# Kernel optimization log

Hardware: AMD Instinct MI355X
Metric: run time of the kernel (lower is better)

## Reference

```python
import jax, jax.numpy as jnp
import numpy as np
import math

HW = (14, 14)          # spatial token grid
L = HW[0] * HW[1]      # 196 spatial tokens
NUM_HEADS = 12
HEAD_DIM = 64
DIM = NUM_HEADS * HEAD_DIM
STEP_LEN = 4           # extension mode: 4 directions, step_length-1 = 3 entries
NUM_DIR = 4
NUM_ENTRY = STEP_LEN - 1
DE = NUM_DIR * NUM_ENTRY  # 12 table channels


def build_spatial_table() -> np.ndarray:
    """Dense [L, L, NUM_DIR*NUM_ENTRY] aggregation table (extension mode)."""
    Hh, Ww = HW
    table = np.zeros((L, L, DE), dtype=np.float32)
    for rank in range(L):
        h, w = divmod(rank, Ww)
        for step in range(1, STEP_LEN):
            dist = math.exp(-step ** 2 / STEP_LEN ** 2)
            se = step - 1
            top = rank - step * Ww
            bottom = rank + step * Ww
            left = rank - step
            right = rank + step
            if top >= 0:
                table[rank, top, 0 * NUM_ENTRY + se] = dist
            if bottom < L:
                table[rank, bottom, 1 * NUM_ENTRY + se] = dist
            if left >= 0 and left // Ww == h:
                table[rank, left, 2 * NUM_ENTRY + se] = dist
            if right < L and right // Ww == h:
                table[rank, right, 3 * NUM_ENTRY + se] = dist
    return table


def setup_inputs() -> dict:
    key = jax.random.key(0)
    ks = jax.random.split(key, 8)
    B, N = 64, L + 1  # +1 class token (skip=1)
    s_in = 1.0 / math.sqrt(DIM)
    inp = {
        "x": jax.random.normal(ks[0], (B, N, DIM), jnp.float32),
        "qkv_w": jax.random.normal(ks[1], (DIM, 3 * DIM), jnp.float32) * s_in,
        "qkv_b": jnp.zeros((3 * DIM,), jnp.float32),
        "proj_w": jax.random.normal(ks[2], (DIM, DIM), jnp.float32) * s_in,
        "proj_b": jnp.zeros((DIM,), jnp.float32),
        "wq": jax.random.normal(ks[3], (DE, NUM_HEADS), jnp.float32) * 0.02,
        "wk": jax.random.normal(ks[4], (DE, NUM_HEADS), jnp.float32) * 0.02,
        "wv": jax.random.normal(ks[5], (DE, NUM_HEADS), jnp.float32) * 0.02,
        "spatial_table": jnp.asarray(build_spatial_table()),
    }
    return inp


def _save_aggregate(v, table, w):
    """SAVE aggregation for one of q/k/v.

    v: [B, H, N, hd] with class token at position 0 (skipped).
    table: [L, L, DE] sparse positional aggregation weights.
    w: [DE, H] per-head channel mixing weights.
    Anchor buffer is identity -> residual add of the spatial tokens.
    """
    cls_tok, sp = v[:, :, :1, :], v[:, :, 1:, :]        # [B,H,1,hd], [B,H,L,hd]
    table_h = jnp.einsum('ije,eh->hij', table, w)       # [H, L, L]
    agg = sp + jnp.einsum('hij,bhjd->bhid', table_h, sp)
    return jnp.concatenate([cls_tok, agg], axis=2)


def reference(x, qkv_w, qkv_b, proj_w, proj_b, wq, wk, wv, spatial_table):
    B, N, C = x.shape
    H, hd = NUM_HEADS, HEAD_DIM
    scale = hd ** -0.5
    qkv = (x @ qkv_w + qkv_b).reshape(B, N, 3, H, hd)
    q, k, v = (jnp.transpose(qkv[:, :, i], (0, 2, 1, 3)) for i in range(3))  # [B,H,N,hd]
    q = _save_aggregate(q, spatial_table, wq)
    k = _save_aggregate(k, spatial_table, wk)
    v = _save_aggregate(v, spatial_table, wv)
    attn = jax.nn.softmax(jnp.einsum('bhid,bhjd->bhij', q, k) * scale, axis=-1)
    out = jnp.einsum('bhij,bhjd->bhid', attn, v)        # [B,H,N,hd]
    out = jnp.transpose(out, (0, 2, 1, 3)).reshape(B, N, C)
    return out @ proj_w + proj_b
```

## Files before the change

### kernel.cpp

```cpp
#include <hip/hip_runtime.h>

typedef unsigned short u16;
typedef __attribute__((ext_vector_type(8))) short short8;
typedef __attribute__((ext_vector_type(4))) float f32x4;

__device__ __forceinline__ u16 f2bf(float f) {
  unsigned u = __builtin_bit_cast(unsigned, f);
  u += 0x7FFFu + ((u >> 16) & 1u);
  return (u16)(u >> 16);
}
__device__ __forceinline__ float bf2f(u16 s) {
  unsigned u = ((unsigned)s) << 16;
  return __builtin_bit_cast(float, u);
}
__device__ __forceinline__ void gll16(const u16* g, u16* l) {
  __builtin_amdgcn_global_load_lds(
      (const __attribute__((address_space(1))) void*)g,
      (__attribute__((address_space(3))) void*)l, 16, 0, 0);
}

__global__ __launch_bounds__(256) void convert_f32_bf16(
    const float* __restrict__ in, u16* __restrict__ out, int n4) {
  int i = blockIdx.x * 256 + threadIdx.x;
  if (i >= n4) return;
  float4 v = ((const float4*)in)[i];
  ushort4 o;
  o.x = f2bf(v.x); o.y = f2bf(v.y); o.z = f2bf(v.z); o.w = f2bf(v.w);
  ((ushort4*)out)[i] = o;
}

__global__ __launch_bounds__(256) void transpose_f32_bf16(
    const float* __restrict__ in, u16* __restrict__ out, int R, int C) {
  __shared__ float tile[32][33];
  int c0 = blockIdx.x * 32, r0 = blockIdx.y * 32;
  int tx = threadIdx.x, ty = threadIdx.y;
  #pragma unroll
  for (int i = 0; i < 32; i += 8)
    tile[ty + i][tx] = in[(size_t)(r0 + ty + i) * C + c0 + tx];
  __syncthreads();
  #pragma unroll
  for (int i = 0; i < 32; i += 8)
    out[(size_t)(c0 + ty + i) * R + r0 + tx] = f2bf(tile[tx][ty + i]);
}

template<int MODE>
__global__ __launch_bounds__(256) void gemm_gll(
    const u16* __restrict__ A, const u16* __restrict__ Bt, int M, int NT,
    const float* __restrict__ bias, u16* __restrict__ ob, float* __restrict__ of) {
  constexpr int K = 768;
  __shared__ __align__(16) u16 Al[128 * 32];
  __shared__ __align__(16) u16 Bl[128 * 32];
  int tid = threadIdx.x, lane = tid & 63, w = tid >> 6;
  int nwg = gridDim.x, orig = blockIdx.x;
  int q = nwg >> 3, r = nwg & 7, xcd = orig & 7, slot = orig >> 3;
  int wg = (xcd < r ? xcd * (q + 1) : r * (q + 1) + (xcd - r) * q) + slot;
  int mt = wg / NT, nt = wg - mt * NT;
  int m0 = mt * 128, n0 = nt * 128;
  int wm = w >> 1, wn = w & 1;
  int lq = lane & 15, oct = lane >> 4;
  int srow = lane >> 2;
  int scol = (lane & 3) << 3;
  int ar0 = m0 + w * 16 + srow;      if (ar0 > M - 1) ar0 = M - 1;
  int ar1 = m0 + 64 + w * 16 + srow; if (ar1 > M - 1) ar1 = M - 1;
  const u16* ga0 = A + (size_t)ar0 * K + scol;
  const u16* ga1 = A + (size_t)ar1 * K + scol;
  const u16* gb0 = Bt + (size_t)(n0 + w * 16 + srow) * K + scol;
  const u16* gb1 = Bt + (size_t)(n0 + 64 + w * 16 + srow) * K + scol;
  u16* la0 = Al + w * 512;
  u16* la1 = Al + 2048 + w * 512;
  u16* lb0 = Bl + w * 512;
  u16* lb1 = Bl + 2048 + w * 512;
  f32x4 acc[4][4] = {};
  for (int kt = 0; kt < K; kt += 32) {
    gll16(ga0 + kt, la0);
    gll16(ga1 + kt, la1);
    gll16(gb0 + kt, lb0);
    gll16(gb1 + kt, lb1);
    __syncthreads();
    short8 af[4], bq[4];
    #pragma unroll
    for (int i = 0; i < 4; ++i)
      af[i] = *(const short8*)(Al + (wm * 64 + i * 16 + lq) * 32 + oct * 8);
    #pragma unroll
    for (int j = 0; j < 4; ++j)
      bq[j] = *(const short8*)(Bl + (wn * 64 + j * 16 + lq) * 32 + oct * 8);
    #pragma unroll
    for (int i = 0; i < 4; ++i)
      #pragma unroll
      for (int j = 0; j < 4; ++j)
        acc[i][j] = __builtin_amdgcn_mfma_f32_16x16x32_bf16(af[i], bq[j], acc[i][j], 0, 0, 0);
    __syncthreads();
  }
  int ldc = NT * 128;
  float bs[4];
  #pragma unroll
  for (int j = 0; j < 4; ++j) bs[j] = bias[n0 + wn * 64 + j * 16 + lq];
  #pragma unroll
  for (int i = 0; i < 4; ++i) {
    #pragma unroll
    for (int rr = 0; rr < 4; ++rr) {
      int m = m0 + wm * 64 + i * 16 + oct * 4 + rr;
      if (m < M) {
        #pragma unroll
        for (int j = 0; j < 4; ++j) {
          int c = n0 + wn * 64 + j * 16 + lq;
          float val = acc[i][j][rr] + bs[j];
          if (MODE == 0) ob[(size_t)m * ldc + c] = f2bf(val);
          else           of[(size_t)m * ldc + c] = val;
        }
      }
    }
  }
}

__global__ __launch_bounds__(256) void save_agg_fused(
    const u16* __restrict__ in, u16* __restrict__ q2, u16* __restrict__ k2,
    u16* __restrict__ v2, const float* __restrict__ wq,
    const float* __restrict__ wk, const float* __restrict__ wv) {
  constexpr int PER = 768 * 197 * 8;
  int vid = blockIdx.x * 256 + threadIdx.x;
  if (vid >= 3 * PER) return;
  int which = vid / PER;
  int rem = vid - which * PER;
  int dv = rem & 7;
  int n = (rem >> 3) % 197;
  int bh = rem / (197 * 8);
  int b = bh / 12, h = bh - b * 12;
  const float* w = (which == 0) ? wq : (which == 1) ? wk : wv;
  u16* outp = (which == 0) ? q2 : (which == 1) ? k2 : v2;
  size_t colbase = (size_t)which * 768 + h * 64 + dv * 8;
  const u16* rowp = in + (size_t)b * 197 * 2304 + colbase;
  size_t rowoff_out = ((size_t)bh * 197 + n) * 64 + dv * 8;
  uint4 cu = *(const uint4*)(rowp + (size_t)n * 2304);
  if (n == 0) { *(uint4*)(outp + rowoff_out) = cu; return; }
  union V8 { uint4 u; u16 s[8]; };
  V8 cv; cv.u = cu;
  float acc[8];
  #pragma unroll
  for (int j = 0; j < 8; ++j) acc[j] = bf2f(cv.s[j]);
  int rank = n - 1;
  int rw = rank % 14;
  const float dist[3] = {0.93941306281347579f, 0.77880078307140487f, 0.56978282473092302f};
  auto add = [&](int ntok, float wt) {
    V8 nv; nv.u = *(const uint4*)(rowp + (size_t)ntok * 2304);
    #pragma unroll
    for (int j = 0; j < 8; ++j) acc[j] += wt * bf2f(nv.s[j]);
  };
  #pragma unroll
  for (int s = 1; s <= 3; ++s) {
    float ds = dist[s - 1];
    if (rank - 14 * s >= 0)  add(n - 14 * s, ds * w[(0 + (s - 1)) * 12 + h]);
    if (rank + 14 * s < 196) add(n + 14 * s, ds * w[(3 + (s - 1)) * 12 + h]);
    if (rw - s >= 0)         add(n - s,      ds * w[(6 + (s - 1)) * 12 + h]);
    if (rw + s <= 13)        add(n + s,      ds * w[(9 + (s - 1)) * 12 + h]);
  }
  V8 ov;
  #pragma unroll
  for (int j = 0; j < 8; ++j) ov.s[j] = f2bf(acc[j]);
  *(uint4*)(outp + rowoff_out) = ov.u;
}

__global__ __launch_bounds__(256) void attn_kernel(
    const u16* __restrict__ q2, const u16* __restrict__ k2,
    const u16* __restrict__ v2, u16* __restrict__ attn_o) {
  __shared__ __align__(16) u16 Vt[64][232];
  __shared__ __align__(16) u16 Pl[4][16][40];
  int bh = blockIdx.x;
  int b = bh / 12, h = bh - b * 12;
  int tid = threadIdx.x, lane = tid & 63, wvid = tid >> 6;
  int lq = lane & 15, oct = lane >> 4;
  const u16* kb_ = k2 + (size_t)bh * 197 * 64;
  const u16* vb_ = v2 + (size_t)bh * 197 * 64;
  const u16* qb_ = q2 + (size_t)bh * 197 * 64;

  for (int idx = tid; idx < 224 * 8; idx += 256) {
    int r = idx >> 3, dv = idx & 7;
    union { uint4 u; u16 s[8]; } val;
    val.u = make_uint4(0, 0, 0, 0);
    if (r < 197) val.u = *(const uint4*)(vb_ + (size_t)r * 64 + dv * 8);
    #pragma unroll
    for (int j = 0; j < 8; ++j) Vt[dv * 8 + j][r] = val.s[j];
  }
  __syncthreads();

  for (int rt = wvid; rt < 13; rt += 4) {
    int qrow = rt * 16 + lq; if (qrow > 196) qrow = 196;
    short8 qa0 = *(const short8*)(qb_ + (size_t)qrow * 64 + oct * 8);
    short8 qa1 = *(const short8*)(qb_ + (size_t)qrow * 64 + 32 + oct * 8);
    f32x4 s[13];
    #pragma unroll
    for (int ct = 0; ct < 13; ++ct) {
      int krow = ct * 16 + lq; if (krow > 196) krow = 196;
      short8 k0 = *(const short8*)(kb_ + (size_t)krow * 64 + oct * 8);
      short8 k1 = *(const short8*)(kb_ + (size_t)krow * 64 + 32 + oct * 8);
      f32x4 a = {0.f, 0.f, 0.f, 0.f};
      a = __builtin_amdgcn_mfma_f32_16x16x32_bf16(qa0, k0, a, 0, 0, 0);
      a = __builtin_amdgcn_mfma_f32_16x16x32_bf16(qa1, k1, a, 0, 0, 0);
      s[ct] = a;
    }
    float m[4] = {-3e38f, -3e38f, -3e38f, -3e38f};
    #pragma unroll
    for (int ct = 0; ct < 13; ++ct) {
      #pragma unroll
      for (int rr = 0; rr < 4; ++rr) {
        float v = s[ct][rr] * 0.125f;
        if (ct == 12 && lq >= 5) v = -1e30f;
        s[ct][rr] = v;
        m[rr] = fmaxf(m[rr], v);
      }
    }
    #pragma unroll
    for (int x = 1; x <= 8; x <<= 1) {
      #pragma unroll
      for (int rr = 0; rr < 4; ++rr) m[rr] = fmaxf(m[rr], __shfl_xor(m[rr], x, 64));
    }
    float rs[4] = {0.f, 0.f, 0.f, 0.f};
    #pragma unroll
    for (int ct = 0; ct < 13; ++ct) {
      #pragma unroll
      for (int rr = 0; rr < 4; ++rr) {
        float e = exp2f((s[ct][rr] - m[rr]) * 1.4426950408889634f);
        float er = bf2f(f2bf(e));
        s[ct][rr] = er;
        rs[rr] += er;
      }
    }
    #pragma unroll
    for (int x = 1; x <= 8; x <<= 1) {
      #pragma unroll
      for (int rr = 0; rr < 4; ++rr) rs[rr] += __shfl_xor(rs[rr], x, 64);
    }
    f32x4 oacc[4];
    #pragma unroll
    for (int dt = 0; dt < 4; ++dt) oacc[dt] = (f32x4){0.f, 0.f, 0.f, 0.f};
    #pragma unroll
    for (int ks = 0; ks < 7; ++ks) {
      #pragma unroll
      for (int tt = 0; tt < 2; ++tt) {
        int ct = ks * 2 + tt;
        #pragma unroll
        for (int rr = 0; rr < 4; ++rr) {
          u16 pu = 0;
          if (ct < 13) pu = f2bf(s[ct < 13 ? ct : 0][rr]);
          Pl[wvid][oct * 4 + rr][tt * 16 + lq] = pu;
        }
      }
      short8 pa = *(const short8*)(&Pl[wvid][lq][oct * 8]);
      #pragma unroll
      for (int dt = 0; dt < 4; ++dt) {
        short8 vbf = *(const short8*)(&Vt[dt * 16 + lq][ks * 32 + oct * 8]);
        oacc[dt] = __builtin_amdgcn_mfma_f32_16x16x32_bf16(pa, vbf, oacc[dt], 0, 0, 0);
      }
    }
    #pragma unroll
    for (int dt = 0; dt < 4; ++dt) {
      #pragma unroll
      for (int rr = 0; rr < 4; ++rr) {
        int qr = rt * 16 + oct * 4 + rr;
        if (qr < 197) {
          float val = oacc[dt][rr] / rs[rr];
          attn_o[(((size_t)b * 197 + qr) * 12 + h) * 64 + dt * 16 + lq] = f2bf(val);
        }
      }
    }
  }
}

extern "C" void kernel_launch(void* const* d_in, const int* in_sizes, int n_in,
                              void* d_out, int out_size, void* d_ws, size_t ws_size,
                              hipStream_t stream) {
  const float* x      = (const float*)d_in[0];
  const float* qkv_w  = (const float*)d_in[1];
  const float* qkv_b  = (const float*)d_in[2];
  const float* proj_w = (const float*)d_in[3];
  const float* proj_b = (const float*)d_in[4];
  const float* wq     = (const float*)d_in[5];
  const float* wk     = (const float*)d_in[6];
  const float* wv     = (const float*)d_in[7];
  float* out = (float*)d_out;

  constexpr size_t SZ = 9682944;
  u16* ws = (u16*)d_ws;
  u16* xb   = ws;
  u16* wT   = xb + SZ;
  u16* pT   = wT + 2304 * 768;
  u16* qkvb = pT + 768 * 768;
  u16* q2   = qkvb + 3 * SZ;
  u16* k2   = q2 + SZ;
  u16* v2   = k2 + SZ;
  u16* ao   = xb;

  convert_f32_bf16<<<dim3(9456), dim3(256), 0, stream>>>(x, xb, 2420736);
  transpose_f32_bf16<<<dim3(72, 24), dim3(32, 8), 0, stream>>>(qkv_w, wT, 768, 2304);
  transpose_f32_bf16<<<dim3(24, 24), dim3(32, 8), 0, stream>>>(proj_w, pT, 768, 768);
  gemm_gll<0><<<dim3(99 * 18), dim3(256), 0, stream>>>(xb, wT, 12608, 18, qkv_b, qkvb, nullptr);
  save_agg_fused<<<dim3(14184), dim3(256), 0, stream>>>(qkvb, q2, k2, v2, wq, wk, wv);
  attn_kernel<<<dim3(768), dim3(256), 0, stream>>>(q2, k2, v2, ao);
  gemm_gll<1><<<dim3(99 * 6), dim3(256), 0, stream>>>(ao, pT, 12608, 6, proj_b, nullptr, out);
}
```

Measured before the change: 303.9 us.

## Widen GEMM K-tile with XOR-swizzled LDS and double attention waves per block

The GEMM now stages a 64-wide K slice per iteration with an XOR-swizzled LDS layout, which halves the number of barriers and should avoid bank conflicts on the fragment reads. The attention kernel moves to 512 threads (8 waves), so each wave handles at most two query row tiles, and it issues the first Q fragment load before the V transpose. This trades more LDS per GEMM block and higher register pressure in attention for better latency hiding and fewer sync points.

```diff
diff --git a/kernel.cpp b/kernel.cpp
--- a/kernel.cpp
+++ b/kernel.cpp
@@ -48,8 +48,8 @@
     const u16* __restrict__ A, const u16* __restrict__ Bt, int M, int NT,
     const float* __restrict__ bias, u16* __restrict__ ob, float* __restrict__ of) {
   constexpr int K = 768;
-  __shared__ __align__(16) u16 Al[128 * 32];
-  __shared__ __align__(16) u16 Bl[128 * 32];
+  __shared__ __align__(16) u16 Al[128 * 64];
+  __shared__ __align__(16) u16 Bl[128 * 64];
   int tid = threadIdx.x, lane = tid & 63, w = tid >> 6;
   int nwg = gridDim.x, orig = blockIdx.x;
   int q = nwg >> 3, r = nwg & 7, xcd = orig & 7, slot = orig >> 3;
@@ -58,37 +58,40 @@
   int m0 = mt * 128, n0 = nt * 128;
   int wm = w >> 1, wn = w & 1;
   int lq = lane & 15, oct = lane >> 4;
-  int srow = lane >> 2;
-  int scol = (lane & 3) << 3;
-  int ar0 = m0 + w * 16 + srow;      if (ar0 > M - 1) ar0 = M - 1;
-  int ar1 = m0 + 64 + w * 16 + srow; if (ar1 > M - 1) ar1 = M - 1;
-  const u16* ga0 = A + (size_t)ar0 * K + scol;
-  const u16* ga1 = A + (size_t)ar1 * K + scol;
-  const u16* gb0 = Bt + (size_t)(n0 + w * 16 + srow) * K + scol;
-  const u16* gb1 = Bt + (size_t)(n0 + 64 + w * 16 + srow) * K + scol;
-  u16* la0 = Al + w * 512;
-  u16* la1 = Al + 2048 + w * 512;
-  u16* lb0 = Bl + w * 512;
-  u16* lb1 = Bl + 2048 + w * 512;
+  int srow = w * 8 + (lane >> 3);
+  int sslot = (lane & 7) ^ (lane >> 3);
+  const u16* gA[4];
+  const u16* gB[4];
+  #pragma unroll
+  for (int p = 0; p < 4; ++p) {
+    int ar = m0 + p * 32 + srow; if (ar > M - 1) ar = M - 1;
+    gA[p] = A + (size_t)ar * K + sslot * 8;
+    gB[p] = Bt + (size_t)(n0 + p * 32 + srow) * K + sslot * 8;
+  }
   f32x4 acc[4][4] = {};
-  for (int kt = 0; kt < K; kt += 32) {
-    gll16(ga0 + kt, la0);
-    gll16(ga1 + kt, la1);
-    gll16(gb0 + kt, lb0);
-    gll16(gb1 + kt, lb1);
+  for (int kt = 0; kt < K; kt += 64) {
+    #pragma unroll
+    for (int p = 0; p < 4; ++p) {
+      gll16(gA[p] + kt, Al + p * 2048 + w * 512);
+      gll16(gB[p] + kt, Bl + p * 2048 + w * 512);
+    }
     __syncthreads();
-    short8 af[4], bq[4];
-    #pragma unroll
-    for (int i = 0; i < 4; ++i)
-      af[i] = *(const short8*)(Al + (wm * 64 + i * 16 + lq) * 32 + oct * 8);
-    #pragma unroll
-    for (int j = 0; j < 4; ++j)
-      bq[j] = *(const short8*)(Bl + (wn * 64 + j * 16 + lq) * 32 + oct * 8);
-    #pragma unroll
-    for (int i = 0; i < 4; ++i)
+    #pragma unroll
+    for (int ks = 0; ks < 2; ++ks) {
+      short8 af[4], bq[4];
+      int rslot = ((ks * 4 + oct) ^ (lq & 7)) * 8;
+      #pragma unroll
+      for (int i = 0; i < 4; ++i)
+        af[i] = *(const short8*)(Al + (wm * 64 + i * 16 + lq) * 64 + rslot);
       #pragma unroll
       for (int j = 0; j < 4; ++j)
-        acc[i][j] = __builtin_amdgcn_mfma_f32_16x16x32_bf16(af[i], bq[j], acc[i][j], 0, 0, 0);
+        bq[j] = *(const short8*)(Bl + (wn * 64 + j * 16 + lq) * 64 + rslot);
+      #pragma unroll
+      for (int i = 0; i < 4; ++i)
+        #pragma unroll
+        for (int j = 0; j < 4; ++j)
+          acc[i][j] = __builtin_amdgcn_mfma_f32_16x16x32_bf16(af[i], bq[j], acc[i][j], 0, 0, 0);
+    }
     __syncthreads();
   }
   int ldc = NT * 128;
@@ -160,11 +163,11 @@
   *(uint4*)(outp + rowoff_out) = ov.u;
 }
 
-__global__ __launch_bounds__(256) void attn_kernel(
+__global__ __launch_bounds__(512) void attn_kernel(
     const u16* __restrict__ q2, const u16* __restrict__ k2,
     const u16* __restrict__ v2, u16* __restrict__ attn_o) {
   __shared__ __align__(16) u16 Vt[64][232];
-  __shared__ __align__(16) u16 Pl[4][16][40];
+  __shared__ __align__(16) u16 Pl[8][16][40];
   int bh = blockIdx.x;
   int b = bh / 12, h = bh - b * 12;
   int tid = threadIdx.x, lane = tid & 63, wvid = tid >> 6;
@@ -173,20 +176,7 @@
   const u16* vb_ = v2 + (size_t)bh * 197 * 64;
   const u16* qb_ = q2 + (size_t)bh * 197 * 64;
 
-  for (int idx = tid; idx < 224 * 8; idx += 256) {
-    int r = idx >> 3, dv = idx & 7;
-    union { uint4 u; u16 s[8]; } val;
-    val.u = make_uint4(0, 0, 0, 0);
-    if (r < 197) val.u = *(const uint4*)(vb_ + (size_t)r * 64 + dv * 8);
-    #pragma unroll
-    for (int j = 0; j < 8; ++j) Vt[dv * 8 + j][r] = val.s[j];
-  }
-  __syncthreads();
-
-  for (int rt = wvid; rt < 13; rt += 4) {
-    int qrow = rt * 16 + lq; if (qrow > 196) qrow = 196;
-    short8 qa0 = *(const short8*)(qb_ + (size_t)qrow * 64 + oct * 8);
-    short8 qa1 = *(const short8*)(qb_ + (size_t)qrow * 64 + 32 + oct * 8);
+  auto process = [&](int rt, short8 qa0, short8 qa1) {
     f32x4 s[13];
     #pragma unroll
     for (int ct = 0; ct < 13; ++ct) {
@@ -263,6 +253,30 @@
         }
       }
     }
+  };
+
+  int rt0 = wvid;
+  int qrow0 = rt0 * 16 + lq; if (qrow0 > 196) qrow0 = 196;
+  short8 qa0 = *(const short8*)(qb_ + (size_t)qrow0 * 64 + oct * 8);
+  short8 qa1 = *(const short8*)(qb_ + (size_t)qrow0 * 64 + 32 + oct * 8);
+
+  for (int idx = tid; idx < 224 * 8; idx += 512) {
+    int rrow = idx >> 3, dv = idx & 7;
+    union { uint4 u; u16 s[8]; } val;
+    val.u = make_uint4(0, 0, 0, 0);
+    if (rrow < 197) val.u = *(const uint4*)(vb_ + (size_t)rrow * 64 + dv * 8);
+    #pragma unroll
+    for (int j = 0; j < 8; ++j) Vt[dv * 8 + j][rrow] = val.s[j];
+  }
+  __syncthreads();
+
+  process(rt0, qa0, qa1);
+  int rt1 = wvid + 8;
+  if (rt1 < 13) {
+    int qrow1 = rt1 * 16 + lq; if (qrow1 > 196) qrow1 = 196;
+    short8 qb0 = *(const short8*)(qb_ + (size_t)qrow1 * 64 + oct * 8);
+    short8 qb1 = *(const short8*)(qb_ + (size_t)qrow1 * 64 + 32 + oct * 8);
+    process(rt1, qb0, qb1);
   }
 }
 
@@ -295,6 +309,6 @@
   transpose_f32_bf16<<<dim3(24, 24), dim3(32, 8), 0, stream>>>(proj_w, pT, 768, 768);
   gemm_gll<0><<<dim3(99 * 18), dim3(256), 0, stream>>>(xb, wT, 12608, 18, qkv_b, qkvb, nullptr);
   save_agg_fused<<<dim3(14184), dim3(256), 0, stream>>>(qkvb, q2, k2, v2, wq, wk, wv);
-  attn_kernel<<<dim3(768), dim3(256), 0, stream>>>(q2, k2, v2, ao);
+  attn_kernel<<<dim3(768), dim3(512), 0, stream>>>(q2, k2, v2, ao);
   gemm_gll<1><<<dim3(99 * 6), dim3(256), 0, stream>>>(ao, pT, 12608, 6, proj_b, nullptr, out);
 }
```

Result: slower. 317.5 us (+4.5%).
